# Optimization experiments

Hardware: AMD Instinct MI355X
Metric: run time of the kernel (lower is better)

## Reference

```python
import jax, jax.numpy as jnp
import numpy as np

NUM_ENVS = 16384
NUM_AGENTS = 16
IN_DIM = 128
GCN_H = 64
RNN_H = 64
E_PER_GRAPH = 128
N_FEAT = 4   # num_individual_actions_features
N_CAT = 8    # num_action_categories
OUT_DIM = NUM_AGENTS * N_FEAT * N_CAT


def setup_inputs() -> dict:
    key = jax.random.key(0)
    ks = jax.random.split(key, 10)
    x = jax.random.normal(ks[0], (NUM_ENVS, NUM_AGENTS, IN_DIM), dtype=jnp.float32)
    edge_index = jax.random.randint(ks[1], (NUM_ENVS, 2, E_PER_GRAPH), 0, NUM_AGENTS, dtype=jnp.int64)
    prev_h = jax.random.normal(ks[2], (NUM_ENVS, NUM_AGENTS, RNN_H), dtype=jnp.float32)
    s = 0.05
    W_gcn = jax.random.normal(ks[3], (IN_DIM, GCN_H), dtype=jnp.float32) * s
    b_gcn = jnp.zeros((GCN_H,), dtype=jnp.float32)
    W_ih = jax.random.normal(ks[4], (3 * RNN_H, GCN_H), dtype=jnp.float32) * s
    W_hh = jax.random.normal(ks[5], (3 * RNN_H, RNN_H), dtype=jnp.float32) * s
    b_ih = jax.random.normal(ks[6], (3 * RNN_H,), dtype=jnp.float32) * s
    b_hh = jax.random.normal(ks[7], (3 * RNN_H,), dtype=jnp.float32) * s
    W_lin = jax.random.normal(ks[8], (OUT_DIM, NUM_AGENTS * RNN_H), dtype=jnp.float32) * s
    b_lin = jax.random.normal(ks[9], (OUT_DIM,), dtype=jnp.float32) * s
    return {"x": x, "edge_index": edge_index, "prev_rnn_hidden_state": prev_h,
            "W_gcn": W_gcn, "b_gcn": b_gcn, "W_ih": W_ih, "W_hh": W_hh,
            "b_ih": b_ih, "b_hh": b_hh, "W_lin": W_lin, "b_lin": b_lin}


def _forward(x, edge_index, prev_h, W_gcn, b_gcn, W_ih, W_hh, b_ih, b_hh, W_lin, b_lin):
    num_envs = x.shape[0]
    N = num_envs * NUM_AGENTS  # flattened node count
    x_flat = x.reshape(N, IN_DIM)

    # block-offset trick: one big disconnected graph
    offsets = (jnp.arange(num_envs, dtype=edge_index.dtype) * NUM_AGENTS)[:, None, None]  # [env,1,1]
    ei = (edge_index + offsets).reshape(num_envs, 2, -1)  # offsets broadcast over [env,2,E]
    row = ei[:, 0, :].reshape(-1)  # source nodes, [env*E]
    col = ei[:, 1, :].reshape(-1)  # target nodes

    # GCNConv: xw = x @ W; add self-loops; sym-normalize; scatter-add to targets
    xw = x_flat @ W_gcn  # [N, GCN_H]
    ones_e = jnp.ones(row.shape[0], dtype=x.dtype)
    deg = jnp.ones((N,), dtype=x.dtype) + jax.ops.segment_sum(ones_e, col, num_segments=N)
    dinv = jax.lax.rsqrt(deg)
    norm = dinv[row] * dinv[col]  # [env*E]
    msg = norm[:, None] * xw[row]  # gather + scale
    agg = jnp.zeros_like(xw).at[col].add(msg)
    agg = agg + xw / deg[:, None]  # self-loop term: 1/deg * xw
    gcn_out = agg + b_gcn  # [N, GCN_H]

    # single-step GRU (torch gate order: r, z, n)
    h = prev_h.reshape(N, RNN_H)
    gx = gcn_out @ W_ih.T + b_ih  # [N, 3H]
    gh = h @ W_hh.T + b_hh
    rx, zx, nx = jnp.split(gx, 3, axis=-1)
    rh, zh, nh = jnp.split(gh, 3, axis=-1)
    r = jax.nn.sigmoid(rx + rh)
    z = jax.nn.sigmoid(zx + zh)
    n = jnp.tanh(nx + r * nh)
    h_new = (1.0 - z) * n + z * h  # [N, H]

    flat = h_new.reshape(num_envs, NUM_AGENTS * RNN_H)
    logits = flat @ W_lin.T + b_lin  # [env, OUT_DIM]
    next_h = h_new.reshape(num_envs, NUM_AGENTS, RNN_H)
    return logits, next_h


def reference(x, edge_index, prev_rnn_hidden_state, W_gcn, b_gcn, W_ih, W_hh, b_ih, b_hh, W_lin, b_lin):
    return _forward(x, edge_index, prev_rnn_hidden_state, W_gcn, b_gcn, W_ih, W_hh, b_ih, b_hh, W_lin, b_lin)
```

## Files before the change

kernel.cpp:

```cpp
#include <hip/hip_runtime.h>
#include <math.h>

namespace {

constexpr int NUM_ENVS = 16384;
constexpr int OUT_DIM = 512;
constexpr int FLAT = 1024;

typedef float floatx4 __attribute__((ext_vector_type(4)));
typedef short shortx8 __attribute__((ext_vector_type(8)));

__device__ __forceinline__ float sigmoidf_(float v) {
    return 1.0f / (1.0f + expf(-v));
}
__device__ __forceinline__ unsigned short f2bf(float f) {
    unsigned int u = __float_as_uint(f);
    u = (u + 0x7FFFu + ((u >> 16) & 1u)) >> 16;
    return (unsigned short)u;
}
__device__ __forceinline__ float bf2f(unsigned short s) {
    return __uint_as_float(((unsigned int)s) << 16);
}
__device__ __forceinline__ shortx8 pack8(const float4& f0, const float4& f1) {
    shortx8 o;
    o[0] = (short)f2bf(f0.x); o[1] = (short)f2bf(f0.y);
    o[2] = (short)f2bf(f0.z); o[3] = (short)f2bf(f0.w);
    o[4] = (short)f2bf(f1.x); o[5] = (short)f2bf(f1.y);
    o[6] = (short)f2bf(f1.z); o[7] = (short)f2bf(f1.w);
    return o;
}

constexpr int WS_FLAG = 0;
constexpr int WS_WGF  = 64;
constexpr int WS_WCF  = WS_WGF + 4096;
constexpr int WS_WLB  = WS_WCF + 12288;
constexpr int WS_GB   = WS_WLB + 262144;

__global__ void prep_kernel(const int* __restrict__ edges_i32,
                            const float* __restrict__ Wg,
                            const float* __restrict__ Wih,
                            const float* __restrict__ Whh,
                            const float* __restrict__ Wlin,
                            float* __restrict__ ws) {
    if (blockIdx.x == 0) {
        __shared__ int any_nonzero;
        if (threadIdx.x == 0) any_nonzero = 0;
        __syncthreads();
        if (threadIdx.x < 128 && edges_i32[2 * threadIdx.x + 1] != 0)
            atomicOr(&any_nonzero, 1);
        __syncthreads();
        if (threadIdx.x == 0) ((int*)ws)[WS_FLAG] = (any_nonzero == 0) ? 1 : 0;
        return;
    }
    const int t = ((int)blockIdx.x - 1) * 256 + (int)threadIdx.x;
    if (t < 8192) {
        const int jj = t & 7, lane = (t >> 3) & 63, slot = t >> 9;
        const int nt = slot >> 2, ks = slot & 3;
        const int n = nt * 16 + (lane & 15);
        const int k = ks * 32 + ((lane >> 4) & 3) * 8 + jj;
        ((unsigned short*)(ws + WS_WGF))[t] = f2bf(Wg[k * 64 + n]);
    } else if (t < 32768) {
        const int u = t - 8192;
        const int jj = u & 7, lane = (u >> 3) & 63, slot = u >> 9;
        const int q8 = ((lane >> 4) & 3) * 8 + jj;
        float val;
        if (slot < 16) {
            const int nt = slot >> 2, ks = slot & 3;
            const int n = nt * 16 + (lane & 15);
            const int k = ks * 32 + q8;
            val = (k < 64) ? Wih[n * 64 + k] : Whh[n * 64 + (k - 64)];
        } else if (slot < 32) {
            const int s = slot - 16, nt = s >> 2, ks = s & 3;
            const int n = 64 + nt * 16 + (lane & 15);
            const int k = ks * 32 + q8;
            val = (k < 64) ? Wih[n * 64 + k] : Whh[n * 64 + (k - 64)];
        } else if (slot < 40) {
            const int s = slot - 32, nt = s >> 1, ks = s & 1;
            const int n = 128 + nt * 16 + (lane & 15);
            val = Wih[n * 64 + ks * 32 + q8];
        } else {
            const int s = slot - 40, nt = s >> 1, ks = s & 1;
            const int n = 128 + nt * 16 + (lane & 15);
            val = Whh[n * 64 + ks * 32 + q8];
        }
        ((unsigned short*)(ws + WS_WCF))[u] = f2bf(val);
    } else if (t < 32768 + 524288) {
        const int u = t - 32768;
        ((unsigned short*)(ws + WS_WLB))[u] = f2bf(Wlin[u]);
    }
}

__global__ __launch_bounds__(256, 3) void gcn_mfma_kernel(
    const float* __restrict__ x,
    const void*  __restrict__ edges,
    const unsigned short* __restrict__ WgF,
    const float* __restrict__ bg,
    unsigned short* __restrict__ gcn,
    const int* __restrict__ flag64)
{
    const int b = blockIdx.x;
    const int tid = threadIdx.x;
    const int lane = tid & 63;
    const int w = tid >> 6;

    __shared__ union {
        unsigned short xbf[64 * 136];
        float xw[64 * 68];
    } U;
    __shared__ int row_s[512];
    __shared__ int col_s[512];
    __shared__ float adj_s[4][16][17];
    __shared__ int deg_s[4][16];
    __shared__ float dinv_s[4][16];
    __shared__ float invdeg_s[4][16];

    {
        float* ap = &adj_s[0][0][0];
        for (int i = tid; i < 4 * 16 * 17; i += 256) ap[i] = 0.0f;
        if (tid < 64) deg_s[tid >> 4][tid & 15] = 0;
    }
    {
        const int r = tid >> 2, q = tid & 3;
        const float4* src = (const float4*)(x + ((size_t)b * 64 + r) * 128 + q * 32);
        unsigned short* dp = &U.xbf[r * 136 + q * 32];
        #pragma unroll
        for (int c = 0; c < 4; ++c) {
            const float4 f0 = src[2 * c], f1 = src[2 * c + 1];
            *(shortx8*)(dp + c * 8) = pack8(f0, f1);
        }
    }
    const bool is64 = (*flag64 != 0);
    #pragma unroll
    for (int t = 0; t < 2; ++t) {
        const int e = tid + 256 * t;
        const int el = e >> 7, idx = e & 127;
        const size_t base = ((size_t)b * 4 + el) * 256;
        int rv, cv;
        if (is64) {
            rv = (int)((const long long*)edges)[base + idx];
            cv = (int)((const long long*)edges)[base + 128 + idx];
        } else {
            rv = ((const int*)edges)[base + idx];
            cv = ((const int*)edges)[base + 128 + idx];
        }
        row_s[e] = rv; col_s[e] = cv;
    }
    __syncthreads();

    #pragma unroll
    for (int t = 0; t < 2; ++t) {
        const int e = tid + 256 * t;
        atomicAdd(&deg_s[e >> 7][col_s[e]], 1);
    }

    shortx8 afr[4];
    #pragma unroll
    for (int ks = 0; ks < 4; ++ks)
        afr[ks] = *(const shortx8*)&U.xbf[(w * 16 + (lane & 15)) * 136 +
                                          ks * 32 + ((lane >> 4) & 3) * 8];
    floatx4 acc[4];
    #pragma unroll
    for (int nt = 0; nt < 4; ++nt) acc[nt] = (floatx4)(0.0f);
    #pragma unroll
    for (int nt = 0; nt < 4; ++nt) {
        #pragma unroll
        for (int ks = 0; ks < 4; ++ks) {
            const shortx8 bfr = *(const shortx8*)&WgF[((nt * 4 + ks) * 64 + lane) * 8];
            acc[nt] = __builtin_amdgcn_mfma_f32_16x16x32_bf16(afr[ks], bfr, acc[nt], 0, 0, 0);
        }
    }
    __syncthreads();

    if (tid < 64) {
        const float d = 1.0f + (float)deg_s[tid >> 4][tid & 15];
        dinv_s[tid >> 4][tid & 15] = rsqrtf(d);
        invdeg_s[tid >> 4][tid & 15] = 1.0f / d;
    }
    #pragma unroll
    for (int nt = 0; nt < 4; ++nt)
        #pragma unroll
        for (int i = 0; i < 4; ++i)
            U.xw[(w * 16 + ((lane >> 4) & 3) * 4 + i) * 68 + nt * 16 + (lane & 15)] = acc[nt][i];
    __syncthreads();

    #pragma unroll
    for (int t = 0; t < 2; ++t) {
        const int e = tid + 256 * t;
        const int el = e >> 7, r = row_s[e], c = col_s[e];
        atomicAdd(&adj_s[el][c][r], dinv_s[el][r] * dinv_s[el][c]);
    }
    if (tid < 64)
        atomicAdd(&adj_s[tid >> 4][tid & 15][tid & 15], invdeg_s[tid >> 4][tid & 15]);
    __syncthreads();

    {
        const int ro = tid >> 2, q = tid & 3;
        const int el = ro >> 4, cl = ro & 15;
        float accs[16];
        #pragma unroll
        for (int m = 0; m < 16; ++m) accs[m] = 0.0f;
        for (int r16 = 0; r16 < 16; ++r16) {
            const float a = adj_s[el][cl][r16];
            const float4* xr = (const float4*)&U.xw[(el * 16 + r16) * 68 + q * 16];
            #pragma unroll
            for (int jq = 0; jq < 4; ++jq) {
                const float4 v = xr[jq];
                accs[4 * jq + 0] += a * v.x;
                accs[4 * jq + 1] += a * v.y;
                accs[4 * jq + 2] += a * v.z;
                accs[4 * jq + 3] += a * v.w;
            }
        }
        unsigned short* dst = gcn + ((size_t)b * 64 + ro) * 64 + q * 16;
        shortx8 o0, o1;
        #pragma unroll
        for (int m = 0; m < 8; ++m) o0[m] = (short)f2bf(accs[m] + bg[q * 16 + m]);
        #pragma unroll
        for (int m = 0; m < 8; ++m) o1[m] = (short)f2bf(accs[8 + m] + bg[q * 16 + 8 + m]);
        *(shortx8*)dst = o0;
        *(shortx8*)(dst + 8) = o1;
    }
}

__global__ __launch_bounds__(256, 2) void gru_mfma_kernel(
    const unsigned short* __restrict__ gcn,
    const float* __restrict__ h_prev,
    const unsigned short* __restrict__ WcF,
    const float* __restrict__ bih,
    const float* __restrict__ bhh,
    float* __restrict__ next_h,
    unsigned short* __restrict__ hb)
{
    const int b = blockIdx.x;
    const int tid = threadIdx.x;
    const int lane = tid & 63;
    const int w = tid >> 6;

    __shared__ unsigned short A_s[64 * 136];
    __shared__ unsigned short W_s[48 * 64 * 8];

    {
        const uint4* src = (const uint4*)WcF;
        uint4* dst = (uint4*)W_s;
        #pragma unroll
        for (int jq = 0; jq < 12; ++jq) dst[tid + 256 * jq] = src[tid + 256 * jq];
    }
    {
        const int r = tid >> 2, q = tid & 3;
        if (q < 2) {
            const uint4* src = (const uint4*)(gcn + ((size_t)b * 64 + r) * 64 + q * 32);
            uint4* dst = (uint4*)&A_s[r * 136 + q * 32];
            #pragma unroll
            for (int jq = 0; jq < 4; ++jq) dst[jq] = src[jq];
        } else {
            const float4* src = (const float4*)(h_prev + ((size_t)b * 64 + r) * 64 + (q - 2) * 32);
            unsigned short* dp = &A_s[r * 136 + 64 + (q - 2) * 32];
            #pragma unroll
            for (int c = 0; c < 4; ++c) {
                const float4 f0 = src[2 * c], f1 = src[2 * c + 1];
                *(shortx8*)(dp + c * 8) = pack8(f0, f1);
            }
        }
    }
    __syncthreads();

    shortx8 afr[4];
    #pragma unroll
    for (int ks = 0; ks < 4; ++ks)
        afr[ks] = *(const shortx8*)&A_s[(w * 16 + (lane & 15)) * 136 +
                                        ks * 32 + ((lane >> 4) & 3) * 8];
    floatx4 aR[4], aZ[4], aNX[4], aNH[4];
    #pragma unroll
    for (int nt = 0; nt < 4; ++nt) {
        aR[nt] = (floatx4)(0.0f); aZ[nt] = (floatx4)(0.0f);
        aNX[nt] = (floatx4)(0.0f); aNH[nt] = (floatx4)(0.0f);
    }
    #pragma unroll
    for (int nt = 0; nt < 4; ++nt) {
        #pragma unroll
        for (int ks = 0; ks < 4; ++ks) {
            const shortx8 bfr = *(const shortx8*)&W_s[((nt * 4 + ks) * 64 + lane) * 8];
            aR[nt] = __builtin_amdgcn_mfma_f32_16x16x32_bf16(afr[ks], bfr, aR[nt], 0, 0, 0);
        }
        #pragma unroll
        for (int ks = 0; ks < 4; ++ks) {
            const shortx8 bfr = *(const shortx8*)&W_s[((16 + nt * 4 + ks) * 64 + lane) * 8];
            aZ[nt] = __builtin_amdgcn_mfma_f32_16x16x32_bf16(afr[ks], bfr, aZ[nt], 0, 0, 0);
        }
        #pragma unroll
        for (int ks = 0; ks < 2; ++ks) {
            const shortx8 bfr = *(const shortx8*)&W_s[((32 + nt * 2 + ks) * 64 + lane) * 8];
            aNX[nt] = __builtin_amdgcn_mfma_f32_16x16x32_bf16(afr[ks], bfr, aNX[nt], 0, 0, 0);
        }
        #pragma unroll
        for (int ks = 0; ks < 2; ++ks) {
            const shortx8 bfr = *(const shortx8*)&W_s[((40 + nt * 2 + ks) * 64 + lane) * 8];
            aNH[nt] = __builtin_amdgcn_mfma_f32_16x16x32_bf16(afr[ks + 2], bfr, aNH[nt], 0, 0, 0);
        }
    }

    const int cl = lane & 15;
    const int rq = (lane >> 4) & 3;
    #pragma unroll
    for (int tp = 0; tp < 4; ++tp) {
        const int f = tp * 16 + cl;
        const float br = bih[f] + bhh[f];
        const float bz = bih[64 + f] + bhh[64 + f];
        const float bnx = bih[128 + f];
        const float bnh = bhh[128 + f];
        #pragma unroll
        for (int i = 0; i < 4; ++i) {
            const int rl = w * 16 + rq * 4 + i;
            const size_t row = (size_t)b * 64 + rl;
            const float hp = bf2f(A_s[rl * 136 + 64 + f]);
            const float r = sigmoidf_(aR[tp][i] + br);
            const float z = sigmoidf_(aZ[tp][i] + bz);
            const float n = tanhf(aNX[tp][i] + bnx + r * (aNH[tp][i] + bnh));
            const float hv = (1.0f - z) * n + z * hp;
            next_h[row * 64 + f] = hv;
            hb[row * 64 + f] = f2bf(hv);
        }
    }
}

__global__ __launch_bounds__(256, 4) void logits_mfma_kernel(
    const unsigned short* __restrict__ A,
    const unsigned short* __restrict__ B,
    const float* __restrict__ bias,
    float* __restrict__ C)
{
    __shared__ __align__(16) unsigned short As[128 * 64];
    __shared__ __align__(16) unsigned short Bs[128 * 64];

    const int tid = threadIdx.x;
    const int lane = tid & 63;
    const int wave = tid >> 6;
    const int wr = wave >> 1;
    const int wc = wave & 1;
    const int m0 = blockIdx.y * 128;
    const int n0 = blockIdx.x * 128;
    const int lr = tid >> 3;
    const int lk = tid & 7;

    floatx4 acc[4][4];
    #pragma unroll
    for (int i = 0; i < 4; ++i)
        #pragma unroll
        for (int jn = 0; jn < 4; ++jn)
            acc[i][jn] = (floatx4)(0.0f);

    for (int kt = 0; kt < 16; ++kt) {
        const int k0 = kt * 64;
        __syncthreads();
        #pragma unroll
        for (int i = 0; i < 4; ++i) {
            const int r = lr + 32 * i;
            const uint4 va = *(const uint4*)&A[(size_t)(m0 + r) * FLAT + k0 + lk * 8];
            *(uint4*)&As[r * 64 + ((lk ^ (r & 7)) * 8)] = va;
            const uint4 vb = *(const uint4*)&B[(size_t)(n0 + r) * FLAT + k0 + lk * 8];
            *(uint4*)&Bs[r * 64 + ((lk ^ (r & 7)) * 8)] = vb;
        }
        __syncthreads();
        #pragma unroll
        for (int s = 0; s < 2; ++s) {
            const int kg = s * 4 + (lane >> 4);
            const int sw = (kg ^ (lane & 7)) * 8;
            shortx8 af[4], bf[4];
            #pragma unroll
            for (int t = 0; t < 4; ++t) {
                af[t] = *(const shortx8*)&As[(wr * 64 + t * 16 + (lane & 15)) * 64 + sw];
                bf[t] = *(const shortx8*)&Bs[(wc * 64 + t * 16 + (lane & 15)) * 64 + sw];
            }
            #pragma unroll
            for (int mt = 0; mt < 4; ++mt)
                #pragma unroll
                for (int nt = 0; nt < 4; ++nt)
                    acc[mt][nt] = __builtin_amdgcn_mfma_f32_16x16x32_bf16(
                        af[mt], bf[nt], acc[mt][nt], 0, 0, 0);
        }
    }

    const int col_l = lane & 15;
    const int rg = lane >> 4;
    #pragma unroll
    for (int nt = 0; nt < 4; ++nt) {
        const int col = n0 + wc * 64 + nt * 16 + col_l;
        const float bv = bias[col];
        #pragma unroll
        for (int mt = 0; mt < 4; ++mt) {
            const int row = m0 + wr * 64 + mt * 16 + rg * 4;
            #pragma unroll
            for (int i = 0; i < 4; ++i) {
                C[(size_t)(row + i) * OUT_DIM + col] = acc[mt][nt][i] + bv;
            }
        }
    }
}

}

extern "C" void kernel_launch(void* const* d_in, const int* in_sizes, int n_in,
                              void* d_out, int out_size, void* d_ws, size_t ws_size,
                              hipStream_t stream) {
    const float* x    = (const float*)d_in[0];
    const void*  ei   = d_in[1];
    const float* h0   = (const float*)d_in[2];
    const float* Wg   = (const float*)d_in[3];
    const float* bg   = (const float*)d_in[4];
    const float* Wih  = (const float*)d_in[5];
    const float* Whh  = (const float*)d_in[6];
    const float* bih  = (const float*)d_in[7];
    const float* bhh  = (const float*)d_in[8];
    const float* Wlin = (const float*)d_in[9];
    const float* blin = (const float*)d_in[10];

    float* out = (float*)d_out;
    float* logits = out;
    float* next_h = out + (size_t)NUM_ENVS * OUT_DIM;

    float* wsf = (float*)d_ws;
    int* flag = (int*)(wsf + WS_FLAG);
    unsigned short* WgF = (unsigned short*)(wsf + WS_WGF);
    unsigned short* WcF = (unsigned short*)(wsf + WS_WCF);
    unsigned short* Wlb = (unsigned short*)(wsf + WS_WLB);
    unsigned short* gb  = (unsigned short*)(wsf + WS_GB);

    prep_kernel<<<2177, 256, 0, stream>>>((const int*)ei, Wg, Wih, Whh, Wlin, wsf);
    gcn_mfma_kernel<<<4096, 256, 0, stream>>>(x, ei, WgF, bg, gb, flag);
    gru_mfma_kernel<<<4096, 256, 0, stream>>>(gb, h0, WcF, bih, bhh, next_h, gb);
    dim3 g2(OUT_DIM / 128, NUM_ENVS / 128);
    logits_mfma_kernel<<<g2, 256, 0, stream>>>(gb, Wlb, blin, logits);
}
```

Measured before the change: 429.0 us.

## Fuse GCN and GRU kernels, keeping GCN output in shared memory

```diff
diff --git a/kernel.cpp b/kernel.cpp
--- a/kernel.cpp
+++ b/kernel.cpp
@@ -10,8 +10,13 @@
 typedef float floatx4 __attribute__((ext_vector_type(4)));
 typedef short shortx8 __attribute__((ext_vector_type(8)));
 
-__device__ __forceinline__ float sigmoidf_(float v) {
-    return 1.0f / (1.0f + expf(-v));
+__device__ __forceinline__ float fast_sigmoid(float v) {
+    const float e = __builtin_amdgcn_exp2f(-v * 1.44269504088896340736f);
+    return __builtin_amdgcn_rcpf(1.0f + e);
+}
+__device__ __forceinline__ float fast_tanh(float v) {
+    const float e = __builtin_amdgcn_exp2f(v * 2.88539008177792681472f);
+    return 1.0f - 2.0f * __builtin_amdgcn_rcpf(1.0f + e);
 }
 __device__ __forceinline__ unsigned short f2bf(float f) {
     unsigned int u = __float_as_uint(f);
@@ -90,12 +95,17 @@
     }
 }
 
-__global__ __launch_bounds__(256, 3) void gcn_mfma_kernel(
+__global__ __launch_bounds__(256, 3) void fused_gcn_gru_kernel(
     const float* __restrict__ x,
     const void*  __restrict__ edges,
     const unsigned short* __restrict__ WgF,
     const float* __restrict__ bg,
-    unsigned short* __restrict__ gcn,
+    const float* __restrict__ h_prev,
+    const unsigned short* __restrict__ WcF,
+    const float* __restrict__ bih,
+    const float* __restrict__ bhh,
+    float* __restrict__ next_h,
+    unsigned short* __restrict__ hb,
     const int* __restrict__ flag64)
 {
     const int b = blockIdx.x;
@@ -103,17 +113,25 @@
     const int lane = tid & 63;
     const int w = tid >> 6;
 
-    __shared__ union {
-        unsigned short xbf[64 * 136];
-        float xw[64 * 68];
-    } U;
-    __shared__ int row_s[512];
-    __shared__ int col_s[512];
+    __shared__ float xw_s[64 * 68];
+    __shared__ unsigned short A_s[64 * 136];
+    __shared__ int rc_s[512];
     __shared__ float adj_s[4][16][17];
     __shared__ int deg_s[4][16];
     __shared__ float dinv_s[4][16];
     __shared__ float invdeg_s[4][16];
 
+    const int ar = w * 16 + (lane & 15);
+    const int aq = (lane >> 4) & 3;
+
+    float4 xf[4][2];
+    #pragma unroll
+    for (int ks = 0; ks < 4; ++ks) {
+        const float4* p = (const float4*)(x + ((size_t)b * 64 + ar) * 128 + ks * 32 + aq * 8);
+        xf[ks][0] = p[0];
+        xf[ks][1] = p[1];
+    }
+
     {
         float* ap = &adj_s[0][0][0];
         for (int i = tid; i < 4 * 16 * 17; i += 256) ap[i] = 0.0f;
@@ -121,13 +139,11 @@
     }
     {
         const int r = tid >> 2, q = tid & 3;
-        const float4* src = (const float4*)(x + ((size_t)b * 64 + r) * 128 + q * 32);
-        unsigned short* dp = &U.xbf[r * 136 + q * 32];
-        #pragma unroll
-        for (int c = 0; c < 4; ++c) {
-            const float4 f0 = src[2 * c], f1 = src[2 * c + 1];
-            *(shortx8*)(dp + c * 8) = pack8(f0, f1);
-        }
+        const float4* src = (const float4*)(h_prev + ((size_t)b * 64 + r) * 64 + q * 16);
+        const float4 f0 = src[0], f1 = src[1], f2 = src[2], f3 = src[3];
+        unsigned short* dp = &A_s[r * 136 + 64 + q * 16];
+        *(shortx8*)dp = pack8(f0, f1);
+        *(shortx8*)(dp + 8) = pack8(f2, f3);
     }
     const bool is64 = (*flag64 != 0);
     #pragma unroll
@@ -143,21 +159,19 @@
             rv = ((const int*)edges)[base + idx];
             cv = ((const int*)edges)[base + 128 + idx];
         }
-        row_s[e] = rv; col_s[e] = cv;
+        rc_s[e] = rv | (cv << 8);
     }
     __syncthreads();
 
     #pragma unroll
     for (int t = 0; t < 2; ++t) {
         const int e = tid + 256 * t;
-        atomicAdd(&deg_s[e >> 7][col_s[e]], 1);
+        atomicAdd(&deg_s[e >> 7][(rc_s[e] >> 8) & 15], 1);
     }
 
     shortx8 afr[4];
     #pragma unroll
-    for (int ks = 0; ks < 4; ++ks)
-        afr[ks] = *(const shortx8*)&U.xbf[(w * 16 + (lane & 15)) * 136 +
-                                          ks * 32 + ((lane >> 4) & 3) * 8];
+    for (int ks = 0; ks < 4; ++ks) afr[ks] = pack8(xf[ks][0], xf[ks][1]);
     floatx4 acc[4];
     #pragma unroll
     for (int nt = 0; nt < 4; ++nt) acc[nt] = (floatx4)(0.0f);
@@ -180,13 +194,14 @@
     for (int nt = 0; nt < 4; ++nt)
         #pragma unroll
         for (int i = 0; i < 4; ++i)
-            U.xw[(w * 16 + ((lane >> 4) & 3) * 4 + i) * 68 + nt * 16 + (lane & 15)] = acc[nt][i];
+            xw_s[(w * 16 + aq * 4 + i) * 68 + nt * 16 + (lane & 15)] = acc[nt][i];
     __syncthreads();
 
     #pragma unroll
     for (int t = 0; t < 2; ++t) {
         const int e = tid + 256 * t;
-        const int el = e >> 7, r = row_s[e], c = col_s[e];
+        const int el = e >> 7;
+        const int r = rc_s[e] & 15, c = (rc_s[e] >> 8) & 15;
         atomicAdd(&adj_s[el][c][r], dinv_s[el][r] * dinv_s[el][c]);
     }
     if (tid < 64)
@@ -201,7 +216,7 @@
         for (int m = 0; m < 16; ++m) accs[m] = 0.0f;
         for (int r16 = 0; r16 < 16; ++r16) {
             const float a = adj_s[el][cl][r16];
-            const float4* xr = (const float4*)&U.xw[(el * 16 + r16) * 68 + q * 16];
+            const float4* xr = (const float4*)&xw_s[(el * 16 + r16) * 68 + q * 16];
             #pragma unroll
             for (int jq = 0; jq < 4; ++jq) {
                 const float4 v = xr[jq];
@@ -211,7 +226,7 @@
                 accs[4 * jq + 3] += a * v.w;
             }
         }
-        unsigned short* dst = gcn + ((size_t)b * 64 + ro) * 64 + q * 16;
+        unsigned short* dst = &A_s[ro * 136 + q * 16];
         shortx8 o0, o1;
         #pragma unroll
         for (int m = 0; m < 8; ++m) o0[m] = (short)f2bf(accs[m] + bg[q * 16 + m]);
@@ -220,55 +235,12 @@
         *(shortx8*)dst = o0;
         *(shortx8*)(dst + 8) = o1;
     }
-}
-
-__global__ __launch_bounds__(256, 2) void gru_mfma_kernel(
-    const unsigned short* __restrict__ gcn,
-    const float* __restrict__ h_prev,
-    const unsigned short* __restrict__ WcF,
-    const float* __restrict__ bih,
-    const float* __restrict__ bhh,
-    float* __restrict__ next_h,
-    unsigned short* __restrict__ hb)
-{
-    const int b = blockIdx.x;
-    const int tid = threadIdx.x;
-    const int lane = tid & 63;
-    const int w = tid >> 6;
-
-    __shared__ unsigned short A_s[64 * 136];
-    __shared__ unsigned short W_s[48 * 64 * 8];
-
-    {
-        const uint4* src = (const uint4*)WcF;
-        uint4* dst = (uint4*)W_s;
-        #pragma unroll
-        for (int jq = 0; jq < 12; ++jq) dst[tid + 256 * jq] = src[tid + 256 * jq];
-    }
-    {
-        const int r = tid >> 2, q = tid & 3;
-        if (q < 2) {
-            const uint4* src = (const uint4*)(gcn + ((size_t)b * 64 + r) * 64 + q * 32);
-            uint4* dst = (uint4*)&A_s[r * 136 + q * 32];
-            #pragma unroll
-            for (int jq = 0; jq < 4; ++jq) dst[jq] = src[jq];
-        } else {
-            const float4* src = (const float4*)(h_prev + ((size_t)b * 64 + r) * 64 + (q - 2) * 32);
-            unsigned short* dp = &A_s[r * 136 + 64 + (q - 2) * 32];
-            #pragma unroll
-            for (int c = 0; c < 4; ++c) {
-                const float4 f0 = src[2 * c], f1 = src[2 * c + 1];
-                *(shortx8*)(dp + c * 8) = pack8(f0, f1);
-            }
-        }
-    }
     __syncthreads();
 
-    shortx8 afr[4];
+    shortx8 gfr[4];
     #pragma unroll
     for (int ks = 0; ks < 4; ++ks)
-        afr[ks] = *(const shortx8*)&A_s[(w * 16 + (lane & 15)) * 136 +
-                                        ks * 32 + ((lane >> 4) & 3) * 8];
+        gfr[ks] = *(const shortx8*)&A_s[ar * 136 + ks * 32 + aq * 8];
     floatx4 aR[4], aZ[4], aNX[4], aNH[4];
     #pragma unroll
     for (int nt = 0; nt < 4; ++nt) {
@@ -279,31 +251,31 @@
     for (int nt = 0; nt < 4; ++nt) {
         #pragma unroll
         for (int ks = 0; ks < 4; ++ks) {
-            const shortx8 bfr = *(const shortx8*)&W_s[((nt * 4 + ks) * 64 + lane) * 8];
-            aR[nt] = __builtin_amdgcn_mfma_f32_16x16x32_bf16(afr[ks], bfr, aR[nt], 0, 0, 0);
+            const shortx8 bfr = *(const shortx8*)&WcF[((nt * 4 + ks) * 64 + lane) * 8];
+            aR[nt] = __builtin_amdgcn_mfma_f32_16x16x32_bf16(gfr[ks], bfr, aR[nt], 0, 0, 0);
         }
         #pragma unroll
         for (int ks = 0; ks < 4; ++ks) {
-            const shortx8 bfr = *(const shortx8*)&W_s[((16 + nt * 4 + ks) * 64 + lane) * 8];
-            aZ[nt] = __builtin_amdgcn_mfma_f32_16x16x32_bf16(afr[ks], bfr, aZ[nt], 0, 0, 0);
+            const shortx8 bfr = *(const shortx8*)&WcF[((16 + nt * 4 + ks) * 64 + lane) * 8];
+            aZ[nt] = __builtin_amdgcn_mfma_f32_16x16x32_bf16(gfr[ks], bfr, aZ[nt], 0, 0, 0);
         }
         #pragma unroll
         for (int ks = 0; ks < 2; ++ks) {
-            const shortx8 bfr = *(const shortx8*)&W_s[((32 + nt * 2 + ks) * 64 + lane) * 8];
-            aNX[nt] = __builtin_amdgcn_mfma_f32_16x16x32_bf16(afr[ks], bfr, aNX[nt], 0, 0, 0);
+            const shortx8 bfr = *(const shortx8*)&WcF[((32 + nt * 2 + ks) * 64 + lane) * 8];
+            aNX[nt] = __builtin_amdgcn_mfma_f32_16x16x32_bf16(gfr[ks], bfr, aNX[nt], 0, 0, 0);
         }
         #pragma unroll
         for (int ks = 0; ks < 2; ++ks) {
-            const shortx8 bfr = *(const shortx8*)&W_s[((40 + nt * 2 + ks) * 64 + lane) * 8];
-            aNH[nt] = __builtin_amdgcn_mfma_f32_16x16x32_bf16(afr[ks + 2], bfr, aNH[nt], 0, 0, 0);
-        }
-    }
-
-    const int cl = lane & 15;
+            const shortx8 bfr = *(const shortx8*)&WcF[((40 + nt * 2 + ks) * 64 + lane) * 8];
+            aNH[nt] = __builtin_amdgcn_mfma_f32_16x16x32_bf16(gfr[ks + 2], bfr, aNH[nt], 0, 0, 0);
+        }
+    }
+
+    const int cl2 = lane & 15;
     const int rq = (lane >> 4) & 3;
     #pragma unroll
     for (int tp = 0; tp < 4; ++tp) {
-        const int f = tp * 16 + cl;
+        const int f = tp * 16 + cl2;
         const float br = bih[f] + bhh[f];
         const float bz = bih[64 + f] + bhh[64 + f];
         const float bnx = bih[128 + f];
@@ -313,9 +285,9 @@
             const int rl = w * 16 + rq * 4 + i;
             const size_t row = (size_t)b * 64 + rl;
             const float hp = bf2f(A_s[rl * 136 + 64 + f]);
-            const float r = sigmoidf_(aR[tp][i] + br);
-            const float z = sigmoidf_(aZ[tp][i] + bz);
-            const float n = tanhf(aNX[tp][i] + bnx + r * (aNH[tp][i] + bnh));
+            const float r = fast_sigmoid(aR[tp][i] + br);
+            const float z = fast_sigmoid(aZ[tp][i] + bz);
+            const float n = fast_tanh(aNX[tp][i] + bnx + r * (aNH[tp][i] + bnh));
             const float hv = (1.0f - z) * n + z * hp;
             next_h[row * 64 + f] = hv;
             hb[row * 64 + f] = f2bf(hv);
@@ -426,8 +398,8 @@
     unsigned short* gb  = (unsigned short*)(wsf + WS_GB);
 
     prep_kernel<<<2177, 256, 0, stream>>>((const int*)ei, Wg, Wih, Whh, Wlin, wsf);
-    gcn_mfma_kernel<<<4096, 256, 0, stream>>>(x, ei, WgF, bg, gb, flag);
-    gru_mfma_kernel<<<4096, 256, 0, stream>>>(gb, h0, WcF, bih, bhh, next_h, gb);
+    fused_gcn_gru_kernel<<<4096, 256, 0, stream>>>(x, ei, WgF, bg, h0, WcF, bih, bhh,
+                                                   next_h, gb, flag);
     dim3 g2(OUT_DIM / 128, NUM_ENVS / 128);
     logits_mfma_kernel<<<g2, 256, 0, stream>>>(gb, Wlb, blin, logits);
 }
```

Result: faster. 396.7 us (-7.5%).
